# Kernel optimization log

Measured on AMD Instinct MI355X. Metric: run time of the kernel, lower is better.

## Reference

```python
import jax, jax.numpy as jnp
import numpy as np

# edge types: (src_node_type, dst_node_type); 0='s', 1='t'
EDGE_TYPES = ((0, 0), (1, 1), (0, 1), (1, 0))
NEG_SLOPE = 0.2


def _conv_single(xb, eidxb, ewb, proj_w, proj_b, q, klin_w, klin_b,
                 lin_src, lin_dst, eproj_w, eproj_b, agg_w, agg_b, att_w, att_b):
    # xb: [2N, C]; eidxb: [4, 2, E]; ewb: [4, E, 1]
    N = xb.shape[0] // 2
    # per-node-type projection (heads=1 so [N, C])
    xn = jnp.stack([xb[:N] @ proj_w[0] + proj_b[0],
                    xb[N:] @ proj_w[1] + proj_b[1]])  # [2, N, C]
    outs = [[], []]  # per destination node type
    for et, (s_t, d_t) in enumerate(EDGE_TYPES):
        src, dst = eidxb[et, 0], eidxb[et, 1]          # [E]
        xsrc, xdst = xn[s_t], xn[d_t]                  # [N, C]
        a_src = (xsrc * lin_src[et]).sum(-1)           # [N]
        a_dst = (xdst * lin_dst[et]).sum(-1)           # [N]
        ewp = ewb[et] @ eproj_w[et] + eproj_b[et]      # [E, C]
        xj, xi = xsrc[src], xdst[dst]                  # gather: [E, C]
        alpha = jax.nn.leaky_relu(a_src[src] + a_dst[dst], NEG_SLOPE)  # [E]
        att = jnp.concatenate([xj, xi, ewp], axis=-1) @ att_w[et] + att_b[et]  # [E, C]
        # segment softmax over destination neighborhoods
        m = jax.ops.segment_max(alpha, dst, num_segments=N)
        e = jnp.exp(alpha - m[dst])
        denom = jax.ops.segment_sum(e, dst, num_segments=N)
        a = e / denom[dst]                              # [E]
        aggr = jax.ops.segment_sum(xj * a[:, None] * att, dst, num_segments=N)  # [N, C]
        upd = jax.nn.relu(jnp.concatenate([aggr, xdst], axis=-1) @ agg_w[et] + agg_b[et])
        outs[d_t].append(jnp.tanh(upd))
    # semantic attention fusion across edge types (group)
    res = []
    for nt in (0, 1):
        o = jnp.stack(outs[nt])  # [T, N, C]
        score = (q[nt] * jnp.tanh(o @ klin_w[nt] + klin_b[nt]).mean(1)).sum(-1)  # [T]
        attn = jax.nn.softmax(score, axis=0)
        res.append((attn[:, None, None] * o).sum(0))  # [N, C]
    return jnp.concatenate(res, axis=0)  # [2N, C]


def setup_inputs() -> dict:
    key = jax.random.key(0)
    B, N, C, E, T = 2, 5000, 128, 65536, 4
    ks = jax.random.split(key, 20)
    w = lambda k, shp, fan: jax.random.normal(k, shp, dtype=jnp.float32) / np.sqrt(fan)
    return {
        'x': jax.random.normal(ks[0], (B, 2 * N, C), dtype=jnp.float32),
        'eidx': jax.random.randint(ks[1], (T, B, 2, E), 0, N, dtype=jnp.int32),
        'ew': jax.random.uniform(ks[2], (T, B, E, 1), dtype=jnp.float32),
        'proj_w': w(ks[3], (2, C, C), C),
        'proj_b': w(ks[4], (2, C), C),
        'q': w(ks[5], (2, C), C),
        'klin_w': w(ks[6], (2, C, C), C),
        'klin_b': w(ks[7], (2, C), C),
        'lin_src': w(ks[8], (T, C), C),
        'lin_dst': w(ks[9], (T, C), C),
        'eproj_w': w(ks[10], (T, 1, C), 1),
        'eproj_b': w(ks[11], (T, C), 1),
        'agg_w': w(ks[12], (T, 2 * C, C), 2 * C),
        'agg_b': w(ks[13], (T, C), 2 * C),
        'att_w': w(ks[14], (T, 3 * C, C), 3 * C),
        'att_b': w(ks[15], (T, C), 3 * C),
    }


def reference(x, eidx, ew, proj_w, proj_b, q, klin_w, klin_b, lin_src, lin_dst,
              eproj_w, eproj_b, agg_w, agg_b, att_w, att_b):
    f = jax.vmap(_conv_single, in_axes=(0, 1, 1) + (None,) * 13)
    return f(x, eidx, ew, proj_w, proj_b, q, klin_w, klin_b, lin_src, lin_dst,
             eproj_w, eproj_b, agg_w, agg_b, att_w, att_b)
```

## Files before the change

kernel.cpp:

```cpp
#include <hip/hip_runtime.h>
#include <math.h>

#define B_    2
#define N_    5000
#define C_    128
#define E_    65536
#define T_    4
#define TWO_N 10000
#define EP_   81920


__device__ __forceinline__ unsigned short f2bf(float f) {
    unsigned u = __float_as_uint(f);
    u += 0x7fffu + ((u >> 16) & 1u);
    return (unsigned short)(u >> 16);
}
__device__ __forceinline__ float bf2f(unsigned short h) {
    return __uint_as_float(((unsigned)h) << 16);
}

typedef __attribute__((ext_vector_type(8))) short bfrag;
typedef __attribute__((ext_vector_type(4))) float ffrag;

__device__ __forceinline__ void split8(const float* __restrict__ p, bfrag& hi, bfrag& lo) {
#pragma unroll
    for (int j = 0; j < 8; ++j) {
        float v = p[j];
        unsigned short h = f2bf(v);
        hi[j] = (short)h;
        lo[j] = (short)f2bf(v - bf2f(h));
    }
}

#define SLOT(i) ((size_t)(i) * 16384)

__device__ __forceinline__ void zero_acc(ffrag (&acc)[2][8]) {
#pragma unroll
    for (int h = 0; h < 2; ++h)
#pragma unroll
        for (int t = 0; t < 8; ++t) acc[h][t] = (ffrag){0.f, 0.f, 0.f, 0.f};
}

__device__ __forceinline__ void mfma128(const float* __restrict__ A,
                                        const unsigned short* __restrict__ Whi,
                                        const unsigned short* __restrict__ Wlo,
                                        ffrag (&acc)[2][8], int bx)
{
    const int wave = threadIdx.x >> 6, lane = threadIdx.x & 63;
    const int mloc = lane & 15, quad = lane >> 4;
    const int row0w = bx * 128 + wave * 32;
    int r0 = row0w + mloc;      if (r0 >= N_) r0 = N_ - 1;
    int r1 = row0w + 16 + mloc; if (r1 >= N_) r1 = N_ - 1;
#pragma unroll
    for (int s = 0; s < 4; ++s) {
        bfrag a0h, a0l, a1h, a1l;
        split8(A + (size_t)r0 * C_ + s * 32 + quad * 8, a0h, a0l);
        split8(A + (size_t)r1 * C_ + s * 32 + quad * 8, a1h, a1l);
        const unsigned short* pBh = Whi + ((size_t)s * 512 + lane) * 8;
        const unsigned short* pBl = Wlo + ((size_t)s * 512 + lane) * 8;
#pragma unroll
        for (int t = 0; t < 8; ++t) {
            bfrag bh = *(const bfrag*)(pBh + (size_t)t * 512);
            bfrag bl = *(const bfrag*)(pBl + (size_t)t * 512);
            acc[0][t] = __builtin_amdgcn_mfma_f32_16x16x32_bf16(a0h, bh, acc[0][t], 0, 0, 0);
            acc[0][t] = __builtin_amdgcn_mfma_f32_16x16x32_bf16(a0l, bh, acc[0][t], 0, 0, 0);
            acc[0][t] = __builtin_amdgcn_mfma_f32_16x16x32_bf16(a0h, bl, acc[0][t], 0, 0, 0);
            acc[1][t] = __builtin_amdgcn_mfma_f32_16x16x32_bf16(a1h, bh, acc[1][t], 0, 0, 0);
            acc[1][t] = __builtin_amdgcn_mfma_f32_16x16x32_bf16(a1l, bh, acc[1][t], 0, 0, 0);
            acc[1][t] = __builtin_amdgcn_mfma_f32_16x16x32_bf16(a1h, bl, acc[1][t], 0, 0, 0);
        }
    }
}

__device__ __forceinline__ void mfma64(const float* __restrict__ A,
                                       const unsigned short* __restrict__ Whi,
                                       const unsigned short* __restrict__ Wlo,
                                       ffrag (&acc)[8], int bx)
{
    const int wave = threadIdx.x >> 6, lane = threadIdx.x & 63;
    const int mloc = lane & 15, quad = lane >> 4;
    int r0 = bx * 64 + wave * 16 + mloc; if (r0 >= N_) r0 = N_ - 1;
#pragma unroll
    for (int s = 0; s < 4; ++s) {
        bfrag a0h, a0l;
        split8(A + (size_t)r0 * C_ + s * 32 + quad * 8, a0h, a0l);
        const unsigned short* pBh = Whi + ((size_t)s * 512 + lane) * 8;
        const unsigned short* pBl = Wlo + ((size_t)s * 512 + lane) * 8;
#pragma unroll
        for (int t = 0; t < 8; ++t) {
            bfrag bh = *(const bfrag*)(pBh + (size_t)t * 512);
            bfrag bl = *(const bfrag*)(pBl + (size_t)t * 512);
            acc[t] = __builtin_amdgcn_mfma_f32_16x16x32_bf16(a0h, bh, acc[t], 0, 0, 0);
            acc[t] = __builtin_amdgcn_mfma_f32_16x16x32_bf16(a0l, bh, acc[t], 0, 0, 0);
            acc[t] = __builtin_amdgcn_mfma_f32_16x16x32_bf16(a0h, bl, acc[t], 0, 0, 0);
        }
    }
}

__device__ __forceinline__ void mfma64_bfA(const unsigned short* __restrict__ A,
                                           const unsigned short* __restrict__ Whi,
                                           const unsigned short* __restrict__ Wlo,
                                           ffrag (&acc)[8], int bx)
{
    const int wave = threadIdx.x >> 6, lane = threadIdx.x & 63;
    const int mloc = lane & 15, quad = lane >> 4;
    int r0 = bx * 64 + wave * 16 + mloc; if (r0 >= N_) r0 = N_ - 1;
#pragma unroll
    for (int s = 0; s < 4; ++s) {
        bfrag a0 = *(const bfrag*)(A + (size_t)r0 * C_ + s * 32 + quad * 8);
        const unsigned short* pBh = Whi + ((size_t)s * 512 + lane) * 8;
        const unsigned short* pBl = Wlo + ((size_t)s * 512 + lane) * 8;
#pragma unroll
        for (int t = 0; t < 8; ++t) {
            bfrag bh = *(const bfrag*)(pBh + (size_t)t * 512);
            bfrag bl = *(const bfrag*)(pBl + (size_t)t * 512);
            acc[t] = __builtin_amdgcn_mfma_f32_16x16x32_bf16(a0, bh, acc[t], 0, 0, 0);
            acc[t] = __builtin_amdgcn_mfma_f32_16x16x32_bf16(a0, bl, acc[t], 0, 0, 0);
        }
    }
}

__device__ __forceinline__ void mfma128_half(const float* __restrict__ A,
                                             const unsigned short* __restrict__ Whi,
                                             const unsigned short* __restrict__ Wlo,
                                             ffrag (&acc)[2][4], int bx, int half)
{
    const int wave = threadIdx.x >> 6, lane = threadIdx.x & 63;
    const int mloc = lane & 15, quad = lane >> 4;
    const int row0w = bx * 128 + wave * 32;
    int r0 = row0w + mloc;      if (r0 >= N_) r0 = N_ - 1;
    int r1 = row0w + 16 + mloc; if (r1 >= N_) r1 = N_ - 1;
#pragma unroll
    for (int s = 0; s < 4; ++s) {
        bfrag a0h, a0l, a1h, a1l;
        split8(A + (size_t)r0 * C_ + s * 32 + quad * 8, a0h, a0l);
        split8(A + (size_t)r1 * C_ + s * 32 + quad * 8, a1h, a1l);
        const unsigned short* pBh = Whi + ((size_t)s * 512 + (size_t)half * 256 + lane) * 8;
        const unsigned short* pBl = Wlo + ((size_t)s * 512 + (size_t)half * 256 + lane) * 8;
#pragma unroll
        for (int t = 0; t < 4; ++t) {
            bfrag bh = *(const bfrag*)(pBh + (size_t)t * 512);
            bfrag bl = *(const bfrag*)(pBl + (size_t)t * 512);
            acc[0][t] = __builtin_amdgcn_mfma_f32_16x16x32_bf16(a0h, bh, acc[0][t], 0, 0, 0);
            acc[0][t] = __builtin_amdgcn_mfma_f32_16x16x32_bf16(a0l, bh, acc[0][t], 0, 0, 0);
            acc[0][t] = __builtin_amdgcn_mfma_f32_16x16x32_bf16(a0h, bl, acc[0][t], 0, 0, 0);
            acc[1][t] = __builtin_amdgcn_mfma_f32_16x16x32_bf16(a1h, bh, acc[1][t], 0, 0, 0);
            acc[1][t] = __builtin_amdgcn_mfma_f32_16x16x32_bf16(a1l, bh, acc[1][t], 0, 0, 0);
            acc[1][t] = __builtin_amdgcn_mfma_f32_16x16x32_bf16(a1h, bl, acc[1][t], 0, 0, 0);
        }
    }
}

#define ZN_ 81028

__global__ __launch_bounds__(256) void setup_kernel(
    const float* __restrict__ proj_w, const float* __restrict__ att_w,
    const float* __restrict__ agg_w, const float* __restrict__ klin_w,
    const float* __restrict__ lin_src, const float* __restrict__ lin_dst,
    const float* __restrict__ eproj_w, const float* __restrict__ eproj_b,
    const float* __restrict__ att_b,
    unsigned short* __restrict__ wh, unsigned short* __restrict__ wl,
    unsigned short* __restrict__ lph, unsigned short* __restrict__ lpl,
    float* __restrict__ v1, float* __restrict__ bias_i, int* __restrict__ zbase)
{
    int blk = blockIdx.x;
    if (blk < 160) {
        int wave = threadIdx.x >> 6, lane = threadIdx.x & 63;
        int unit = blk * 4 + wave;
        int id = unit >> 5;
        int st = unit & 31;
        int s = st >> 3, t = st & 7;
        const float* src;
        if (id < 2)       src = proj_w + (size_t)id * 16384;
        else if (id < 6)  src = att_w + (size_t)(id - 2) * 384 * C_;
        else if (id < 10) src = att_w + (size_t)(id - 6) * 384 * C_ + (size_t)128 * C_;
        else if (id < 14) src = agg_w + (size_t)(id - 10) * 256 * C_;
        else if (id < 18) src = agg_w + (size_t)(id - 14) * 256 * C_ + (size_t)128 * C_;
        else              src = klin_w + (size_t)(id - 18) * 16384;
        int mloc = lane & 15, quad = lane >> 4;
        size_t dbase = SLOT(id) + ((size_t)(s * 8 + t) * 64 + lane) * 8;
#pragma unroll
        for (int j = 0; j < 8; ++j) {
            float v = src[(size_t)(s * 32 + quad * 8 + j) * C_ + t * 16 + mloc];
            unsigned short h = f2bf(v);
            wh[dbase + j] = h;
            wl[dbase + j] = f2bf(v - bf2f(h));
        }
    } else if (blk == 160) {
        int s = threadIdx.x >> 6;
        int lane = threadIdx.x & 63;
        int mloc = lane & 15, quad = lane >> 4;
        const float* vec = nullptr;
        if (mloc < 8) {
            int nt = mloc >> 2, idx = mloc & 3;
            if (idx == 0)      vec = lin_src + nt * C_;
            else if (idx == 1) vec = lin_src + (nt + 2) * C_;
            else if (idx == 2) vec = lin_dst + nt * C_;
            else               vec = lin_dst + (3 - nt) * C_;
        }
        size_t dbase = ((size_t)(s * 64) + lane) * 8;
#pragma unroll
        for (int j = 0; j < 8; ++j) {
            float v = vec ? vec[s * 32 + quad * 8 + j] : 0.f;
            unsigned short h = f2bf(v);
            lph[dbase + j] = h;
            lpl[dbase + j] = f2bf(v - bf2f(h));
        }
    } else if (blk < 163) {
        int et = (blk - 161) * 2 + (threadIdx.x >> 7);
        int c = threadIdx.x & 127;
        float s1 = 0.f, s0 = 0.f;
        for (int k = 0; k < 128; ++k) {
            float wv = att_w[(size_t)et * 384 * C_ + (size_t)(256 + k) * C_ + c];
            s1 = fmaf(eproj_w[et * C_ + k], wv, s1);
            s0 = fmaf(eproj_b[et * C_ + k], wv, s0);
        }
        v1[et * C_ + c] = s1;
        bias_i[et * C_ + c] = att_b[et * C_ + c] + s0;
    } else {
        int base = (blk - 163) * 1024 + threadIdx.x * 4;
#pragma unroll
        for (int j = 0; j < 4; ++j)
            if (base + j < ZN_) zbase[base + j] = 0;
    }
}

__global__ __launch_bounds__(256) void cp_kernel(
    const int* __restrict__ eidx, int* __restrict__ count,
    const float* __restrict__ x,
    const unsigned short* __restrict__ wph, const unsigned short* __restrict__ wpl,
    const float* __restrict__ proj_b,
    const float* __restrict__ lin_src, const float* __restrict__ lin_dst,
    float* __restrict__ xn, float* __restrict__ asrc, float* __restrict__ adst)
{
    int blk = blockIdx.x;
    if (blk < 2048) {
        int be = blk & 7;
        int et = be & 3, b = be >> 2;
        int e = (blk >> 3) * 256 + threadIdx.x;
        int dst = eidx[(((size_t)et * B_ + b) * 2 + 1) * E_ + e];
        atomicAdd(&count[(size_t)be * N_ + dst], 1);
        return;
    }
    int pidx = blk - 2048;
    int bx = pidx % 40;
    int nt = (pidx / 40) & 1;
    int b = pidx / 80;
    const float* A = x + ((size_t)b * TWO_N + (size_t)nt * N_) * C_;
    ffrag acc[2][8];
    zero_acc(acc);
    mfma128(A, wph + SLOT(nt), wpl + SLOT(nt), acc, bx);
    float* out = xn + (size_t)(b * 2 + nt) * N_ * C_;
    const float* bias = proj_b + nt * C_;
    const int wave = threadIdx.x >> 6, lane = threadIdx.x & 63;
    const int mloc = lane & 15, quad = lane >> 4;
    const int rbase = bx * 128 + wave * 32 + quad * 4;
    const float* lv0 = lin_src + nt * C_;
    const float* lv1 = lin_src + (2 + nt) * C_;
    const float* lv2 = lin_dst + nt * C_;
    const float* lv3 = lin_dst + (3 - nt) * C_;
    float linv[4][8];
#pragma unroll
    for (int t = 0; t < 8; ++t) {
        int col = t * 16 + mloc;
        linv[0][t] = lv0[col]; linv[1][t] = lv1[col];
        linv[2][t] = lv2[col]; linv[3][t] = lv3[col];
    }
    const int et0 = nt, et1 = 2 + nt, et2 = nt, et3 = 3 - nt;
#pragma unroll
    for (int h = 0; h < 2; ++h)
#pragma unroll
        for (int r = 0; r < 4; ++r) {
            int row = rbase + h * 16 + r;
            bool ok = (row < N_);
            float p0 = 0.f, p1 = 0.f, p2 = 0.f, p3 = 0.f;
#pragma unroll
            for (int t = 0; t < 8; ++t) {
                int col = t * 16 + mloc;
                float vv = acc[h][t][r] + bias[col];
                if (ok) out[(size_t)row * C_ + col] = vv;
                p0 = fmaf(vv, linv[0][t], p0);
                p1 = fmaf(vv, linv[1][t], p1);
                p2 = fmaf(vv, linv[2][t], p2);
                p3 = fmaf(vv, linv[3][t], p3);
            }
#pragma unroll
            for (int m = 1; m < 16; m <<= 1) {
                p0 += __shfl_xor(p0, m);
                p1 += __shfl_xor(p1, m);
                p2 += __shfl_xor(p2, m);
                p3 += __shfl_xor(p3, m);
            }
            if (mloc == 0 && ok) {
                asrc[(size_t)(b * T_ + et0) * N_ + row] = p0;
                asrc[(size_t)(b * T_ + et1) * N_ + row] = p1;
                adst[(size_t)(b * T_ + et2) * N_ + row] = p2;
                adst[(size_t)(b * T_ + et3) * N_ + row] = p3;
            }
        }
}

__global__ __launch_bounds__(256) void scan_kernel(const int* __restrict__ count,
                                                   int* __restrict__ offs,
                                                   unsigned int* __restrict__ pwq)
{
    int be = blockIdx.x;
    const int* cnt = count + (size_t)be * N_;
    int* off = offs + (size_t)be * (N_ + 1);
    __shared__ int sums[256];
    int tid = threadIdx.x;
    const int chunk = (N_ + 255) / 256;
    int lo = tid * chunk, hi = min(lo + chunk, N_);
    int s = 0;
    for (int i = lo; i < hi; ++i) s += (cnt[i] + 3) & ~3;
    sums[tid] = s;
    __syncthreads();
    for (int d = 1; d < 256; d <<= 1) {
        int v = (tid >= d) ? sums[tid - d] : 0;
        __syncthreads();
        sums[tid] += v;
        __syncthreads();
    }
    int run = (tid > 0) ? sums[tid - 1] : 0;
    uint2* ep = (uint2*)pwq;
    for (int i = lo; i < hi; ++i) {
        off[i] = run;
        int c = cnt[i], pc = (c + 3) & ~3;
        for (int k = c; k < pc; ++k)
            ep[(size_t)be * EP_ + run + k] = make_uint2(0u, 0u);
        run += pc;
    }
    if (tid == 255) off[N_] = sums[255];
}

__global__ __launch_bounds__(256) void sy_kernel(
    const int* __restrict__ eidx, const float* __restrict__ ew,
    const float* __restrict__ asrc, const float* __restrict__ adst,
    const int* __restrict__ offs, int* __restrict__ cursor,
    unsigned int* __restrict__ pwq,
    const float* __restrict__ xn,
    const unsigned short* __restrict__ wph, const unsigned short* __restrict__ wpl,
    const float* __restrict__ bias_i,
    unsigned short* __restrict__ G, unsigned short* __restrict__ YiB)
{
    int blk = blockIdx.x;
    if (blk < 2048) {
        int be = blk & 7;
        int et = be & 3, b = be >> 2;
        int e = (blk >> 3) * 256 + threadIdx.x;
        size_t ebase = ((size_t)et * B_ + b) * 2 * E_;
        int src = eidx[ebase + e];
        int dst = eidx[ebase + E_ + e];
        float al = asrc[(size_t)be * N_ + src] + adst[(size_t)be * N_ + dst];
        al = (al > 0.f) ? al : 0.2f * al;
        float p = __expf(al);
        float w = ew[((size_t)et * B_ + b) * E_ + e];
        int pos = offs[(size_t)be * (N_ + 1) + dst] +
                  atomicAdd(&cursor[(size_t)be * N_ + dst], 1);
        unsigned int packed = (unsigned int)src | ((unsigned int)f2bf(p * w) << 16);
        ((uint2*)pwq)[(size_t)be * EP_ + pos] = make_uint2(__float_as_uint(p), packed);
        return;
    }
    int yidx = blk - 2048;
    int be = yidx & 7;
    int et = be & 3, b = be >> 2;
    int rest = yidx >> 3;
    int half = rest & 1;
    int role = (rest >> 1) & 1;
    int bx = rest >> 2;
    int s_t = et & 1, d_t = ((et + 1) >> 1) & 1;
    int ntsel = (role == 0) ? s_t : d_t;
    const float* A = xn + (size_t)(b * 2 + ntsel) * N_ * C_;
    int slot = (role == 0) ? 2 + et : 6 + et;
    ffrag acc[2][4];
#pragma unroll
    for (int h = 0; h < 2; ++h)
#pragma unroll
        for (int t = 0; t < 4; ++t) acc[h][t] = (ffrag){0.f, 0.f, 0.f, 0.f};
    mfma128_half(A, wph + SLOT(slot), wpl + SLOT(slot), acc, bx, half);
    const float* bias = bias_i + et * C_;
    const int wave = threadIdx.x >> 6, lane = threadIdx.x & 63;
    const int mloc = lane & 15, quad = lane >> 4;
    const int rbase = bx * 128 + wave * 32 + quad * 4;
#pragma unroll
    for (int h = 0; h < 2; ++h)
#pragma unroll
        for (int r = 0; r < 4; ++r) {
            int row = rbase + h * 16 + r;
            if (row >= N_) continue;
#pragma unroll
            for (int t = 0; t < 4; ++t) {
                int col = (half * 4 + t) * 16 + mloc;
                float v = acc[h][t][r];
                if (role == 0) {
                    float xv = A[(size_t)row * C_ + col];
                    *(ushort2*)(G + ((size_t)be * N_ + row) * 256 + 2 * col) =
                        make_ushort2(f2bf(v * xv), f2bf(xv));
                } else {
                    YiB[((size_t)be * N_ + row) * C_ + col] = f2bf(v + bias[col]);
                }
            }
        }
}

__global__ __launch_bounds__(256) void aggregate_kernel(
    const unsigned short* __restrict__ G, const unsigned short* __restrict__ YiB,
    const float* __restrict__ v1, const unsigned int* __restrict__ pwq,
    const int* __restrict__ offs, unsigned short* __restrict__ aggrB)
{
    int pair = blockIdx.x & 7;
    int n = (blockIdx.x >> 3) * 4 + (threadIdx.x >> 6);
    int et = pair & 3;
    int be = pair;
    int l = threadIdx.x & 63;
    const unsigned short* Gp = G + (size_t)be * N_ * 256;
    int beg = offs[(size_t)be * (N_ + 1) + n];
    int end = offs[(size_t)be * (N_ + 1) + n + 1];
    const unsigned int* ep = pwq + ((size_t)be * EP_ + beg) * 2;
    float a1x = 0.f, a1y = 0.f, a2x = 0.f, a2y = 0.f, a3x = 0.f, a3y = 0.f, denom = 0.f;
    int cnt = end - beg;
    for (int i = 0; i < cnt; i += 4) {
        uint4 u01 = *(const uint4*)(ep + 2 * i);
        uint4 u23 = *(const uint4*)(ep + 2 * i + 4);
        float p0 = __uint_as_float(u01.x), q0 = bf2f((unsigned short)(u01.y >> 16));
        float p1 = __uint_as_float(u01.z), q1 = bf2f((unsigned short)(u01.w >> 16));
        float p2 = __uint_as_float(u23.x), q2 = bf2f((unsigned short)(u23.y >> 16));
        float p3 = __uint_as_float(u23.z), q3 = bf2f((unsigned short)(u23.w >> 16));
        int s0 = u01.y & 0xffff, s1 = u01.w & 0xffff;
        int s2 = u23.y & 0xffff, s3 = u23.w & 0xffff;
        ushort4 g0 = *(const ushort4*)(Gp + (size_t)s0 * 256 + 4 * l);
        ushort4 g1 = *(const ushort4*)(Gp + (size_t)s1 * 256 + 4 * l);
        ushort4 g2 = *(const ushort4*)(Gp + (size_t)s2 * 256 + 4 * l);
        ushort4 g3 = *(const ushort4*)(Gp + (size_t)s3 * 256 + 4 * l);
        denom += p0 + p1 + p2 + p3;
        a1x = fmaf(p0, bf2f(g0.x), a1x); a2x = fmaf(p0, bf2f(g0.y), a2x);
        a3x = fmaf(q0, bf2f(g0.y), a3x);
        a1y = fmaf(p0, bf2f(g0.z), a1y); a2y = fmaf(p0, bf2f(g0.w), a2y);
        a3y = fmaf(q0, bf2f(g0.w), a3y);
        a1x = fmaf(p1, bf2f(g1.x), a1x); a2x = fmaf(p1, bf2f(g1.y), a2x);
        a3x = fmaf(q1, bf2f(g1.y), a3x);
        a1y = fmaf(p1, bf2f(g1.z), a1y); a2y = fmaf(p1, bf2f(g1.w), a2y);
        a3y = fmaf(q1, bf2f(g1.w), a3y);
        a1x = fmaf(p2, bf2f(g2.x), a1x); a2x = fmaf(p2, bf2f(g2.y), a2x);
        a3x = fmaf(q2, bf2f(g2.y), a3x);
        a1y = fmaf(p2, bf2f(g2.z), a1y); a2y = fmaf(p2, bf2f(g2.w), a2y);
        a3y = fmaf(q2, bf2f(g2.w), a3y);
        a1x = fmaf(p3, bf2f(g3.x), a1x); a2x = fmaf(p3, bf2f(g3.y), a2x);
        a3x = fmaf(q3, bf2f(g3.y), a3x);
        a1y = fmaf(p3, bf2f(g3.z), a1y); a2y = fmaf(p3, bf2f(g3.w), a2y);
        a3y = fmaf(q3, bf2f(g3.w), a3y);
    }
    ushort2 yiu = *(const ushort2*)(YiB + ((size_t)be * N_ + n) * C_ + 2 * l);
    float2 vv = *(const float2*)(v1 + et * C_ + 2 * l);
    float inv = (denom > 0.f) ? 1.f / denom : 0.f;
    float ox = (a1x + bf2f(yiu.x) * a2x + vv.x * a3x) * inv;
    float oy = (a1y + bf2f(yiu.y) * a2y + vv.y * a3y) * inv;
    *(ushort2*)(aggrB + ((size_t)be * N_ + n) * C_ + 2 * l) = make_ushort2(f2bf(ox), f2bf(oy));
}

#define AGGK_BLOCKS 640

__global__ __launch_bounds__(256) void aggklin_kernel(
    const unsigned short* __restrict__ aggrB, const float* __restrict__ xn,
    const unsigned short* __restrict__ wph, const unsigned short* __restrict__ wpl,
    const float* __restrict__ agg_b, const float* __restrict__ klin_b,
    const float* __restrict__ q, unsigned short* __restrict__ outsB,
    float* __restrict__ colsum, int* __restrict__ done, float* __restrict__ attn)
{
    int blk = blockIdx.x;
    int be = blk & 7, bx = blk >> 3;
    int et = be & 3, b = be >> 2;
    int d_t = ((et + 1) >> 1) & 1;
    size_t base = (size_t)be * N_ * C_;
    ffrag acc[8];
#pragma unroll
    for (int t = 0; t < 8; ++t) acc[t] = (ffrag){0.f, 0.f, 0.f, 0.f};
    mfma64_bfA(aggrB + base, wph + SLOT(10 + et), wpl + SLOT(10 + et), acc, bx);
    mfma64(xn + (size_t)(b * 2 + d_t) * N_ * C_, wph + SLOT(14 + et), wpl + SLOT(14 + et),
           acc, bx);
    __shared__ unsigned short tile[64][136];
    const float* bias = agg_b + et * C_;
    const int wave = threadIdx.x >> 6, lane = threadIdx.x & 63;
    const int mloc = lane & 15, quad = lane >> 4;
#pragma unroll
    for (int r = 0; r < 4; ++r) {
        int lrow = wave * 16 + quad * 4 + r;
        int row = bx * 64 + lrow;
#pragma unroll
        for (int t = 0; t < 8; ++t) {
            int col = t * 16 + mloc;
            float v = acc[t][r] + bias[col];
            v = (v > 0.f) ? tanhf(v) : 0.f;
            unsigned short hv = f2bf(v);
            tile[lrow][col] = hv;
            if (row < N_) outsB[base + (size_t)row * C_ + col] = hv;
        }
    }
    __syncthreads();
    int nt = d_t, tt = (et >= 2) ? 1 : 0;
    ffrag acc2[8];
#pragma unroll
    for (int t = 0; t < 8; ++t) acc2[t] = (ffrag){0.f, 0.f, 0.f, 0.f};
    const unsigned short* Kh = wph + SLOT(18 + nt);
    const unsigned short* Kl = wpl + SLOT(18 + nt);
    int lr = wave * 16 + mloc;
#pragma unroll
    for (int s = 0; s < 4; ++s) {
        bfrag a0 = *(const bfrag*)&tile[lr][s * 32 + quad * 8];
        const unsigned short* pBh = Kh + ((size_t)s * 512 + lane) * 8;
        const unsigned short* pBl = Kl + ((size_t)s * 512 + lane) * 8;
#pragma unroll
        for (int t = 0; t < 8; ++t) {
            bfrag bh = *(const bfrag*)(pBh + (size_t)t * 512);
            bfrag bl = *(const bfrag*)(pBl + (size_t)t * 512);
            acc2[t] = __builtin_amdgcn_mfma_f32_16x16x32_bf16(a0, bh, acc2[t], 0, 0, 0);
            acc2[t] = __builtin_amdgcn_mfma_f32_16x16x32_bf16(a0, bl, acc2[t], 0, 0, 0);
        }
    }
    __shared__ float cs[128];
    if (threadIdx.x < 128) cs[threadIdx.x] = 0.f;
    __syncthreads();
    const int rbase = bx * 64 + wave * 16 + quad * 4;
#pragma unroll
    for (int t = 0; t < 8; ++t) {
        int col = t * 16 + mloc;
        float bv = klin_b[nt * C_ + col];
        float s = 0.f;
#pragma unroll
        for (int r = 0; r < 4; ++r) {
            int row = rbase + r;
            if (row < N_) s += tanhf(acc2[t][r] + bv);
        }
        atomicAdd(&cs[col], s);
    }
    __syncthreads();
    if (threadIdx.x < 128)
        atomicAdd(&colsum[(size_t)((b * 2 + nt) * 2 + tt) * C_ + threadIdx.x], cs[threadIdx.x]);
    __shared__ int isLast;
    if (threadIdx.x == 0) {
        __threadfence();
        isLast = (atomicAdd(done, 1) == AGGK_BLOCKS - 1) ? 1 : 0;
    }
    __syncthreads();
    if (!isLast) return;
    __shared__ float red[2][2];
    for (int bnt = 0; bnt < 4; ++bnt) {
        int ntl = bnt & 1;
        float v0 = 0.f, v1l = 0.f;
        if (threadIdx.x < 128) {
            int c = threadIdx.x;
            float qc = q[ntl * C_ + c];
            float c0 = atomicAdd(&colsum[(size_t)(bnt * 2 + 0) * C_ + c], 0.f);
            float c1 = atomicAdd(&colsum[(size_t)(bnt * 2 + 1) * C_ + c], 0.f);
            v0 = qc * c0;
            v1l = qc * c1;
        }
#pragma unroll
        for (int m = 32; m > 0; m >>= 1) {
            v0 += __shfl_down(v0, m);
            v1l += __shfl_down(v1l, m);
        }
        if ((threadIdx.x & 63) == 0 && wave < 2) {
            red[wave][0] = v0;
            red[wave][1] = v1l;
        }
        __syncthreads();
        if (threadIdx.x == 0) {
            float s0 = (red[0][0] + red[1][0]) / (float)N_;
            float s1 = (red[0][1] + red[1][1]) / (float)N_;
            float mx = fmaxf(s0, s1);
            float e0 = __expf(s0 - mx), e1 = __expf(s1 - mx);
            float invd = 1.f / (e0 + e1);
            attn[bnt * 2 + 0] = e0 * invd;
            attn[bnt * 2 + 1] = e1 * invd;
        }
        __syncthreads();
    }
}

__global__ void output_kernel(const unsigned short* __restrict__ outsB,
                              const float* __restrict__ attn,
                              float* __restrict__ out)
{
    int idx = blockIdx.x * blockDim.x + threadIdx.x;
    int c4 = idx & 31;
    int row = idx >> 5;
    int b = row / TWO_N;
    int r = row % TWO_N;
    int nt = (r >= N_) ? 1 : 0;
    int n = r - nt * N_;
    int et0 = nt, et1 = 3 - nt;
    float a0 = attn[(b * 2 + nt) * 2 + 0];
    float a1 = attn[(b * 2 + nt) * 2 + 1];
    const ushort4* o0 = (const ushort4*)(outsB + ((size_t)(b * T_ + et0) * N_ + n) * C_);
    const ushort4* o1 = (const ushort4*)(outsB + ((size_t)(b * T_ + et1) * N_ + n) * C_);
    ushort4 u0 = o0[c4], u1 = o1[c4];
    float4 o;
    o.x = a0 * bf2f(u0.x) + a1 * bf2f(u1.x);
    o.y = a0 * bf2f(u0.y) + a1 * bf2f(u1.y);
    o.z = a0 * bf2f(u0.z) + a1 * bf2f(u1.z);
    o.w = a0 * bf2f(u0.w) + a1 * bf2f(u1.w);
    ((float4*)out)[idx] = o;
}

extern "C" void kernel_launch(void* const* d_in, const int* in_sizes, int n_in,
                              void* d_out, int out_size, void* d_ws, size_t ws_size,
                              hipStream_t stream)
{
    const float* x       = (const float*)d_in[0];
    const int*   eidx    = (const int*)d_in[1];
    const float* ew      = (const float*)d_in[2];
    const float* proj_w  = (const float*)d_in[3];
    const float* proj_b  = (const float*)d_in[4];
    const float* q       = (const float*)d_in[5];
    const float* klin_w  = (const float*)d_in[6];
    const float* klin_b  = (const float*)d_in[7];
    const float* lin_src = (const float*)d_in[8];
    const float* lin_dst = (const float*)d_in[9];
    const float* eproj_w = (const float*)d_in[10];
    const float* eproj_b = (const float*)d_in[11];
    const float* agg_w   = (const float*)d_in[12];
    const float* agg_b   = (const float*)d_in[13];
    const float* att_w   = (const float*)d_in[14];
    const float* att_b   = (const float*)d_in[15];

    float* ws = (float*)d_ws;
    size_t o = 0;
    float* xn     = ws + o; o += 2560000;
    float* GU     = ws + o; o += 5120000;
    float* YiBf   = ws + o; o += 2560000;
    float* aggrBf = ws + o; o += 2560000;
    float* pwqf   = ws + o; o += 2 * 8 * EP_;
    float* asrc   = ws + o; o += 40000;
    float* adst   = ws + o; o += 40000;
    float* v1     = ws + o; o += 512;
    float* bias_i = ws + o; o += 512;
    float* attn   = ws + o; o += 16;
    int*   count  = (int*)(ws + o); o += 40000;
    int*   cursor = (int*)(ws + o); o += 40000;
    float* colsum = ws + o; o += 1024;
    int*   done   = (int*)(ws + o); o += 4;
    int*   offs   = (int*)(ws + o); o += 40008;
    unsigned short* wph = (unsigned short*)(ws + o); o += 163840;
    unsigned short* wpl = (unsigned short*)(ws + o); o += 163840;
    unsigned short* lph = (unsigned short*)(ws + o); o += 1024;
    unsigned short* lpl = (unsigned short*)(ws + o); o += 1024;

    unsigned short* G     = (unsigned short*)GU;
    unsigned short* outsB = (unsigned short*)GU;
    unsigned short* YiB   = (unsigned short*)YiBf;
    unsigned short* aggrB = (unsigned short*)aggrBf;
    unsigned int*   pwq   = (unsigned int*)pwqf;

    setup_kernel<<<dim3(243), 256, 0, stream>>>(proj_w, att_w, agg_w, klin_w,
                                                lin_src, lin_dst, eproj_w, eproj_b,
                                                att_b, wph, wpl, lph, lpl,
                                                v1, bias_i, count);
    cp_kernel<<<dim3(2208), 256, 0, stream>>>(eidx, count, x, wph, wpl, proj_b,
                                              lin_src, lin_dst, xn, asrc, adst);
    scan_kernel<<<dim3(B_ * T_), 256, 0, stream>>>(count, offs, pwq);
    sy_kernel<<<dim3(3328), 256, 0, stream>>>(eidx, ew, asrc, adst, offs, cursor,
                                              pwq, xn, wph, wpl, bias_i, G, YiB);
    aggregate_kernel<<<dim3(10000), 256, 0, stream>>>(G, YiB, v1, pwq, offs, aggrB);
    aggklin_kernel<<<dim3(AGGK_BLOCKS), 256, 0, stream>>>(aggrB, xn, wph, wpl, agg_b,
                                                          klin_b, q, outsB, colsum,
                                                          done, attn);
    output_kernel<<<dim3(2500), 256, 0, stream>>>(outsB, attn, (float*)d_out);
}
```

Baseline: 281.9 us.

## Store projected node features as bf16 and vectorize edge-index loads four per thread

```diff
diff --git a/kernel.cpp b/kernel.cpp
--- a/kernel.cpp
+++ b/kernel.cpp
@@ -72,27 +72,30 @@
     }
 }
 
-__device__ __forceinline__ void mfma64(const float* __restrict__ A,
-                                       const unsigned short* __restrict__ Whi,
-                                       const unsigned short* __restrict__ Wlo,
-                                       ffrag (&acc)[8], int bx)
+__device__ __forceinline__ void mfma128_half_bfA(const unsigned short* __restrict__ A,
+                                                 const unsigned short* __restrict__ Whi,
+                                                 const unsigned short* __restrict__ Wlo,
+                                                 ffrag (&acc)[2][4], int bx, int half)
 {
     const int wave = threadIdx.x >> 6, lane = threadIdx.x & 63;
     const int mloc = lane & 15, quad = lane >> 4;
-    int r0 = bx * 64 + wave * 16 + mloc; if (r0 >= N_) r0 = N_ - 1;
+    const int row0w = bx * 128 + wave * 32;
+    int r0 = row0w + mloc;      if (r0 >= N_) r0 = N_ - 1;
+    int r1 = row0w + 16 + mloc; if (r1 >= N_) r1 = N_ - 1;
 #pragma unroll
     for (int s = 0; s < 4; ++s) {
-        bfrag a0h, a0l;
-        split8(A + (size_t)r0 * C_ + s * 32 + quad * 8, a0h, a0l);
-        const unsigned short* pBh = Whi + ((size_t)s * 512 + lane) * 8;
-        const unsigned short* pBl = Wlo + ((size_t)s * 512 + lane) * 8;
-#pragma unroll
-        for (int t = 0; t < 8; ++t) {
+        bfrag a0 = *(const bfrag*)(A + (size_t)r0 * C_ + s * 32 + quad * 8);
+        bfrag a1 = *(const bfrag*)(A + (size_t)r1 * C_ + s * 32 + quad * 8);
+        const unsigned short* pBh = Whi + ((size_t)s * 512 + (size_t)half * 256 + lane) * 8;
+        const unsigned short* pBl = Wlo + ((size_t)s * 512 + (size_t)half * 256 + lane) * 8;
+#pragma unroll
+        for (int t = 0; t < 4; ++t) {
             bfrag bh = *(const bfrag*)(pBh + (size_t)t * 512);
             bfrag bl = *(const bfrag*)(pBl + (size_t)t * 512);
-            acc[t] = __builtin_amdgcn_mfma_f32_16x16x32_bf16(a0h, bh, acc[t], 0, 0, 0);
-            acc[t] = __builtin_amdgcn_mfma_f32_16x16x32_bf16(a0l, bh, acc[t], 0, 0, 0);
-            acc[t] = __builtin_amdgcn_mfma_f32_16x16x32_bf16(a0h, bl, acc[t], 0, 0, 0);
+            acc[0][t] = __builtin_amdgcn_mfma_f32_16x16x32_bf16(a0, bh, acc[0][t], 0, 0, 0);
+            acc[0][t] = __builtin_amdgcn_mfma_f32_16x16x32_bf16(a0, bl, acc[0][t], 0, 0, 0);
+            acc[1][t] = __builtin_amdgcn_mfma_f32_16x16x32_bf16(a1, bh, acc[1][t], 0, 0, 0);
+            acc[1][t] = __builtin_amdgcn_mfma_f32_16x16x32_bf16(a1, bl, acc[1][t], 0, 0, 0);
         }
     }
 }
@@ -116,37 +119,6 @@
             bfrag bl = *(const bfrag*)(pBl + (size_t)t * 512);
             acc[t] = __builtin_amdgcn_mfma_f32_16x16x32_bf16(a0, bh, acc[t], 0, 0, 0);
             acc[t] = __builtin_amdgcn_mfma_f32_16x16x32_bf16(a0, bl, acc[t], 0, 0, 0);
-        }
-    }
-}
-
-__device__ __forceinline__ void mfma128_half(const float* __restrict__ A,
-                                             const unsigned short* __restrict__ Whi,
-                                             const unsigned short* __restrict__ Wlo,
-                                             ffrag (&acc)[2][4], int bx, int half)
-{
-    const int wave = threadIdx.x >> 6, lane = threadIdx.x & 63;
-    const int mloc = lane & 15, quad = lane >> 4;
-    const int row0w = bx * 128 + wave * 32;
-    int r0 = row0w + mloc;      if (r0 >= N_) r0 = N_ - 1;
-    int r1 = row0w + 16 + mloc; if (r1 >= N_) r1 = N_ - 1;
-#pragma unroll
-    for (int s = 0; s < 4; ++s) {
-        bfrag a0h, a0l, a1h, a1l;
-        split8(A + (size_t)r0 * C_ + s * 32 + quad * 8, a0h, a0l);
-        split8(A + (size_t)r1 * C_ + s * 32 + quad * 8, a1h, a1l);
-        const unsigned short* pBh = Whi + ((size_t)s * 512 + (size_t)half * 256 + lane) * 8;
-        const unsigned short* pBl = Wlo + ((size_t)s * 512 + (size_t)half * 256 + lane) * 8;
-#pragma unroll
-        for (int t = 0; t < 4; ++t) {
-            bfrag bh = *(const bfrag*)(pBh + (size_t)t * 512);
-            bfrag bl = *(const bfrag*)(pBl + (size_t)t * 512);
-            acc[0][t] = __builtin_amdgcn_mfma_f32_16x16x32_bf16(a0h, bh, acc[0][t], 0, 0, 0);
-            acc[0][t] = __builtin_amdgcn_mfma_f32_16x16x32_bf16(a0l, bh, acc[0][t], 0, 0, 0);
-            acc[0][t] = __builtin_amdgcn_mfma_f32_16x16x32_bf16(a0h, bl, acc[0][t], 0, 0, 0);
-            acc[1][t] = __builtin_amdgcn_mfma_f32_16x16x32_bf16(a1h, bh, acc[1][t], 0, 0, 0);
-            acc[1][t] = __builtin_amdgcn_mfma_f32_16x16x32_bf16(a1l, bh, acc[1][t], 0, 0, 0);
-            acc[1][t] = __builtin_amdgcn_mfma_f32_16x16x32_bf16(a1h, bl, acc[1][t], 0, 0, 0);
         }
     }
 }
@@ -231,18 +203,23 @@
     const unsigned short* __restrict__ wph, const unsigned short* __restrict__ wpl,
     const float* __restrict__ proj_b,
     const float* __restrict__ lin_src, const float* __restrict__ lin_dst,
-    float* __restrict__ xn, float* __restrict__ asrc, float* __restrict__ adst)
+    unsigned short* __restrict__ xnB, float* __restrict__ asrc, float* __restrict__ adst)
 {
     int blk = blockIdx.x;
-    if (blk < 2048) {
+    if (blk < 512) {
         int be = blk & 7;
         int et = be & 3, b = be >> 2;
-        int e = (blk >> 3) * 256 + threadIdx.x;
-        int dst = eidx[(((size_t)et * B_ + b) * 2 + 1) * E_ + e];
-        atomicAdd(&count[(size_t)be * N_ + dst], 1);
+        int t4 = (blk >> 3) * 256 + threadIdx.x;
+        size_t ebase = ((size_t)et * B_ + b) * 2 * E_;
+        int4 d4 = *(const int4*)(eidx + ebase + E_ + 4 * t4);
+        int* cp = count + (size_t)be * N_;
+        atomicAdd(&cp[d4.x], 1);
+        atomicAdd(&cp[d4.y], 1);
+        atomicAdd(&cp[d4.z], 1);
+        atomicAdd(&cp[d4.w], 1);
         return;
     }
-    int pidx = blk - 2048;
+    int pidx = blk - 512;
     int bx = pidx % 40;
     int nt = (pidx / 40) & 1;
     int b = pidx / 80;
@@ -250,7 +227,7 @@
     ffrag acc[2][8];
     zero_acc(acc);
     mfma128(A, wph + SLOT(nt), wpl + SLOT(nt), acc, bx);
-    float* out = xn + (size_t)(b * 2 + nt) * N_ * C_;
+    unsigned short* out = xnB + (size_t)(b * 2 + nt) * N_ * C_;
     const float* bias = proj_b + nt * C_;
     const int wave = threadIdx.x >> 6, lane = threadIdx.x & 63;
     const int mloc = lane & 15, quad = lane >> 4;
@@ -278,7 +255,7 @@
             for (int t = 0; t < 8; ++t) {
                 int col = t * 16 + mloc;
                 float vv = acc[h][t][r] + bias[col];
-                if (ok) out[(size_t)row * C_ + col] = vv;
+                if (ok) out[(size_t)row * C_ + col] = f2bf(vv);
                 p0 = fmaf(vv, linv[0][t], p0);
                 p1 = fmaf(vv, linv[1][t], p1);
                 p2 = fmaf(vv, linv[2][t], p2);
@@ -338,30 +315,40 @@
     const float* __restrict__ asrc, const float* __restrict__ adst,
     const int* __restrict__ offs, int* __restrict__ cursor,
     unsigned int* __restrict__ pwq,
-    const float* __restrict__ xn,
+    const unsigned short* __restrict__ xnB,
     const unsigned short* __restrict__ wph, const unsigned short* __restrict__ wpl,
     const float* __restrict__ bias_i,
     unsigned short* __restrict__ G, unsigned short* __restrict__ YiB)
 {
     int blk = blockIdx.x;
-    if (blk < 2048) {
+    if (blk < 512) {
         int be = blk & 7;
         int et = be & 3, b = be >> 2;
-        int e = (blk >> 3) * 256 + threadIdx.x;
+        int t4 = (blk >> 3) * 256 + threadIdx.x;
         size_t ebase = ((size_t)et * B_ + b) * 2 * E_;
-        int src = eidx[ebase + e];
-        int dst = eidx[ebase + E_ + e];
-        float al = asrc[(size_t)be * N_ + src] + adst[(size_t)be * N_ + dst];
-        al = (al > 0.f) ? al : 0.2f * al;
-        float p = __expf(al);
-        float w = ew[((size_t)et * B_ + b) * E_ + e];
-        int pos = offs[(size_t)be * (N_ + 1) + dst] +
-                  atomicAdd(&cursor[(size_t)be * N_ + dst], 1);
-        unsigned int packed = (unsigned int)src | ((unsigned int)f2bf(p * w) << 16);
-        ((uint2*)pwq)[(size_t)be * EP_ + pos] = make_uint2(__float_as_uint(p), packed);
+        int4 s4 = *(const int4*)(eidx + ebase + 4 * t4);
+        int4 d4 = *(const int4*)(eidx + ebase + E_ + 4 * t4);
+        float4 w4 = *(const float4*)(ew + ((size_t)et * B_ + b) * E_ + 4 * t4);
+        const float* ap = asrc + (size_t)be * N_;
+        const float* dp = adst + (size_t)be * N_;
+        const int* op = offs + (size_t)be * (N_ + 1);
+        int* cp = cursor + (size_t)be * N_;
+        uint2* epb = (uint2*)pwq + (size_t)be * EP_;
+#pragma unroll
+        for (int j = 0; j < 4; ++j) {
+            int src = (j == 0) ? s4.x : (j == 1) ? s4.y : (j == 2) ? s4.z : s4.w;
+            int dst = (j == 0) ? d4.x : (j == 1) ? d4.y : (j == 2) ? d4.z : d4.w;
+            float w = (j == 0) ? w4.x : (j == 1) ? w4.y : (j == 2) ? w4.z : w4.w;
+            float al = ap[src] + dp[dst];
+            al = (al > 0.f) ? al : 0.2f * al;
+            float p = __expf(al);
+            int pos = op[dst] + atomicAdd(&cp[dst], 1);
+            unsigned int packed = (unsigned int)src | ((unsigned int)f2bf(p * w) << 16);
+            epb[pos] = make_uint2(__float_as_uint(p), packed);
+        }
         return;
     }
-    int yidx = blk - 2048;
+    int yidx = blk - 512;
     int be = yidx & 7;
     int et = be & 3, b = be >> 2;
     int rest = yidx >> 3;
@@ -370,14 +357,14 @@
     int bx = rest >> 2;
     int s_t = et & 1, d_t = ((et + 1) >> 1) & 1;
     int ntsel = (role == 0) ? s_t : d_t;
-    const float* A = xn + (size_t)(b * 2 + ntsel) * N_ * C_;
+    const unsigned short* A = xnB + (size_t)(b * 2 + ntsel) * N_ * C_;
     int slot = (role == 0) ? 2 + et : 6 + et;
     ffrag acc[2][4];
 #pragma unroll
     for (int h = 0; h < 2; ++h)
 #pragma unroll
         for (int t = 0; t < 4; ++t) acc[h][t] = (ffrag){0.f, 0.f, 0.f, 0.f};
-    mfma128_half(A, wph + SLOT(slot), wpl + SLOT(slot), acc, bx, half);
+    mfma128_half_bfA(A, wph + SLOT(slot), wpl + SLOT(slot), acc, bx, half);
     const float* bias = bias_i + et * C_;
     const int wave = threadIdx.x >> 6, lane = threadIdx.x & 63;
     const int mloc = lane & 15, quad = lane >> 4;
@@ -393,7 +380,7 @@
                 int col = (half * 4 + t) * 16 + mloc;
                 float v = acc[h][t][r];
                 if (role == 0) {
-                    float xv = A[(size_t)row * C_ + col];
+                    float xv = bf2f(A[(size_t)row * C_ + col]);
                     *(ushort2*)(G + ((size_t)be * N_ + row) * 256 + 2 * col) =
                         make_ushort2(f2bf(v * xv), f2bf(xv));
                 } else {
@@ -461,7 +448,7 @@
 #define AGGK_BLOCKS 640
 
 __global__ __launch_bounds__(256) void aggklin_kernel(
-    const unsigned short* __restrict__ aggrB, const float* __restrict__ xn,
+    const unsigned short* __restrict__ aggrB, const unsigned short* __restrict__ xnB,
     const unsigned short* __restrict__ wph, const unsigned short* __restrict__ wpl,
     const float* __restrict__ agg_b, const float* __restrict__ klin_b,
     const float* __restrict__ q, unsigned short* __restrict__ outsB,
@@ -476,8 +463,8 @@
 #pragma unroll
     for (int t = 0; t < 8; ++t) acc[t] = (ffrag){0.f, 0.f, 0.f, 0.f};
     mfma64_bfA(aggrB + base, wph + SLOT(10 + et), wpl + SLOT(10 + et), acc, bx);
-    mfma64(xn + (size_t)(b * 2 + d_t) * N_ * C_, wph + SLOT(14 + et), wpl + SLOT(14 + et),
-           acc, bx);
+    mfma64_bfA(xnB + (size_t)(b * 2 + d_t) * N_ * C_, wph + SLOT(14 + et),
+               wpl + SLOT(14 + et), acc, bx);
     __shared__ unsigned short tile[64][136];
     const float* bias = agg_b + et * C_;
     const int wave = threadIdx.x >> 6, lane = threadIdx.x & 63;
@@ -626,7 +613,7 @@
 
     float* ws = (float*)d_ws;
     size_t o = 0;
-    float* xn     = ws + o; o += 2560000;
+    float* xnBf   = ws + o; o += 1280000;
     float* GU     = ws + o; o += 5120000;
     float* YiBf   = ws + o; o += 2560000;
     float* aggrBf = ws + o; o += 2560000;
@@ -646,6 +633,7 @@
     unsigned short* lph = (unsigned short*)(ws + o); o += 1024;
     unsigned short* lpl = (unsigned short*)(ws + o); o += 1024;
 
+    unsigned short* xnB   = (unsigned short*)xnBf;
     unsigned short* G     = (unsigned short*)GU;
     unsigned short* outsB = (unsigned short*)GU;
     unsigned short* YiB   = (unsigned short*)YiBf;
@@ -656,13 +644,13 @@
                                                 lin_src, lin_dst, eproj_w, eproj_b,
                                                 att_b, wph, wpl, lph, lpl,
                                                 v1, bias_i, count);
-    cp_kernel<<<dim3(2208), 256, 0, stream>>>(eidx, count, x, wph, wpl, proj_b,
-                                              lin_src, lin_dst, xn, asrc, adst);
+    cp_kernel<<<dim3(672), 256, 0, stream>>>(eidx, count, x, wph, wpl, proj_b,
+                                             lin_src, lin_dst, xnB, asrc, adst);
     scan_kernel<<<dim3(B_ * T_), 256, 0, stream>>>(count, offs, pwq);
-    sy_kernel<<<dim3(3328), 256, 0, stream>>>(eidx, ew, asrc, adst, offs, cursor,
-                                              pwq, xn, wph, wpl, bias_i, G, YiB);
+    sy_kernel<<<dim3(1792), 256, 0, stream>>>(eidx, ew, asrc, adst, offs, cursor,
+                                              pwq, xnB, wph, wpl, bias_i, G, YiB);
     aggregate_kernel<<<dim3(10000), 256, 0, stream>>>(G, YiB, v1, pwq, offs, aggrB);
-    aggklin_kernel<<<dim3(AGGK_BLOCKS), 256, 0, stream>>>(aggrB, xn, wph, wpl, agg_b,
+    aggklin_kernel<<<dim3(AGGK_BLOCKS), 256, 0, stream>>>(aggrB, xnB, wph, wpl, agg_b,
                                                           klin_b, q, outsB, colsum,
                                                           done, attn);
     output_kernel<<<dim3(2500), 256, 0, stream>>>(outsB, attn, (float*)d_out);
```

Result: faster. 272.6 us (-3.3%).
